# Kernel optimization log

Hardware: AMD Instinct MI355X
Metric: run time of the kernel (lower is better)

The kernel has to match this reference:

```python
import jax, jax.numpy as jnp
import numpy as np

N = 8192        # nodes (A.shape[0])
D_IN = 128      # input_dim
D_OUT = 128     # output_dim
D_THETA = 256   # hardcoded in GCN_liner_theta_1
DROP_KEEP = 0.8 # DropEdge percent


def setup_inputs() -> dict:
    key = jax.random.key(0)
    ks = jax.random.split(key, 6)
    H = jax.random.normal(ks[0], (N, D_IN), dtype=jnp.float32)
    U = jax.random.uniform(ks[1], (N, N), dtype=jnp.float32)
    upper = jnp.triu((U < 0.01).astype(jnp.float32), 1)
    A_adj = upper + upper.T + jnp.eye(N, dtype=jnp.float32)
    bn_gamma = jnp.ones((D_IN,), jnp.float32)
    bn_beta = jnp.zeros((D_IN,), jnp.float32)
    W_theta = jax.random.normal(ks[2], (D_THETA, D_IN), jnp.float32) * 0.05
    b_theta = jnp.zeros((D_THETA,), jnp.float32)
    W_out = jax.random.normal(ks[3], (D_OUT, D_IN), jnp.float32) * 0.05
    b_out = jnp.zeros((D_OUT,), jnp.float32)
    return {"H": H, "A_adj": A_adj, "bn_gamma": bn_gamma, "bn_beta": bn_beta,
            "W_theta": W_theta, "b_theta": b_theta, "W_out": W_out, "b_out": b_out}


def reference(H, A_adj, bn_gamma, bn_beta, W_theta, b_theta, W_out, b_out):
    n = H.shape[0]
    # BatchNorm1d in training mode: batch stats over the node dimension
    mean = H.mean(axis=0)
    var = H.var(axis=0)  # biased, matches torch training normalization
    Hn = (H - mean) * jax.lax.rsqrt(var + 1e-5) * bn_gamma + bn_beta

    # theta projection -> pairwise euclidean distances
    Hx = Hn @ W_theta.T + b_theta                     # [N, 256]
    sq = jnp.sum(Hx * Hx, axis=1)                     # [N]
    dist = sq[:, None] + sq[None, :] - 2.0 * (Hx @ Hx.T)
    dist = jnp.sqrt(jnp.clip(dist, 1e-12, None))      # [N, N]

    A = jnp.exp(-0.2 * dist)
    A = jnp.clip(jax.nn.sigmoid(A), 0.1, None)
    # DropEdge detaches A in the original (A never carries grad)
    A = jax.lax.stop_gradient(A)

    dkey = jax.random.key(42)
    keep = jax.random.uniform(dkey, (n, n)) < DROP_KEEP
    triu = jnp.triu(jnp.ones((n, n), dtype=bool), 0)
    Bt = jnp.where(triu & keep, A, 0.0)
    B = Bt + Bt.T - jnp.diag(jnp.diag(Bt))

    mask = jnp.ceil(A_adj * 1e-5)
    A2 = B * mask + jnp.eye(n, dtype=B.dtype)
    A3 = jnp.where(A2 > 0.6, A2, 0.0)                 # threshold (host loop in torch)

    # symmetric normalization D^-1/2 A D^-1/2 without dense diag matmuls
    d_inv_sqrt = jax.lax.rsqrt(A3.sum(axis=1))        # diag always >= 1
    A_hat = A3 * d_inv_sqrt[:, None] * d_inv_sqrt[None, :]

    out = A_hat @ (Hn @ W_out.T + b_out)              # [N, D_OUT]
    out = jnp.where(out >= 0, out, 0.01 * out)        # LeakyReLU(0.01)
    return out, A3
```

## Files before the change

### kernel.cpp

```cpp
#include <hip/hip_runtime.h>
#include <cstdint>
#include <cstddef>

#define N 8192
#define DIN 128
#define DTH 256
#define DOUT 128
#define ROWCAP 256
#define LISTCAP 512

__device__ __forceinline__ void threefry_0_42(uint32_t x0, uint32_t x1,
                                              uint32_t& o0, uint32_t& o1) {
  const uint32_t ks0 = 0u;
  const uint32_t ks1 = 42u;
  const uint32_t ks2 = 0x1BD11BDAu ^ 0u ^ 42u;
  x0 += ks0; x1 += ks1;
#define TF_R(r) { x0 += x1; x1 = (x1 << (r)) | (x1 >> (32 - (r))); x1 ^= x0; }
  TF_R(13) TF_R(15) TF_R(26) TF_R(6)
  x0 += ks1; x1 += ks2 + 1u;
  TF_R(17) TF_R(29) TF_R(16) TF_R(24)
  x0 += ks2; x1 += ks0 + 2u;
  TF_R(13) TF_R(15) TF_R(26) TF_R(6)
  x0 += ks0; x1 += ks1 + 3u;
  TF_R(17) TF_R(29) TF_R(16) TF_R(24)
  x0 += ks1; x1 += ks2 + 4u;
  TF_R(13) TF_R(15) TF_R(26) TF_R(6)
  x0 += ks2; x1 += ks0 + 5u;
#undef TF_R
  o0 = x0; o1 = x1;
}

__device__ __forceinline__ bool dropedge_keep(uint32_t t) {
  uint32_t y0, y1;
  threefry_0_42(0u, t, y0, y1);
  uint32_t bits = y0 ^ y1;
  float u = __uint_as_float((bits >> 9) | 0x3f800000u) - 1.0f;
  return u < 0.8f;
}

__global__ __launch_bounds__(256) void k_pre(
    const float* __restrict__ H,
    const float* __restrict__ Wt, const float* __restrict__ bt,
    const float* __restrict__ Wo, const float* __restrict__ bo,
    float* __restrict__ part_s, float* __restrict__ part_s2,
    float* __restrict__ Wc, float* __restrict__ bc,
    float* __restrict__ deg ) {
  int b = blockIdx.x;
  int tid = threadIdx.x;
  if (b < 64) {
    __shared__ float ls[8][DIN];
    __shared__ float ls2[8][DIN];
    int rg = tid >> 5;
    int c4 = tid & 31;
    int rbase = b * 128;
    float s[4] = {0,0,0,0}, s2[4] = {0,0,0,0};
    for (int k = 0; k < 16; ++k) {
      int r = rbase + rg + k * 8;
      float4 h = ((const float4*)(H + (size_t)r * DIN))[c4];
      s[0] += h.x; s2[0] += h.x * h.x;
      s[1] += h.y; s2[1] += h.y * h.y;
      s[2] += h.z; s2[2] += h.z * h.z;
      s[3] += h.w; s2[3] += h.w * h.w;
    }
#pragma unroll
    for (int q = 0; q < 4; ++q) { ls[rg][c4*4+q] = s[q]; ls2[rg][c4*4+q] = s2[q]; }
    __syncthreads();
    if (tid < DIN) {
      float a = 0.f, bb = 0.f;
#pragma unroll
      for (int g = 0; g < 8; ++g) { a += ls[g][tid]; bb += ls2[g][tid]; }
      part_s[b * DIN + tid] = a;
      part_s2[b * DIN + tid] = bb;
    }
  } else if (b < 256) {
    int idx = (b - 64) * 256 + tid;
    int k = idx / 384, c = idx % 384;
    Wc[idx] = (c < 256) ? Wt[(size_t)c * DIN + k] : Wo[(size_t)(c - 256) * DIN + k];
  } else if (b < 258) {
    int c = (b - 256) * 256 + tid;
    if (c < 384) bc[c] = (c < 256) ? bt[c] : bo[c - 256];
  } else {
    int g = (b - 258) * 256 + tid;
    ((int4*)deg)[g] = make_int4(0, 0, 0, 0);
  }
}

__global__ void k_bn_final(const float* __restrict__ part_s,
                           const float* __restrict__ part_s2,
                           const float* __restrict__ gamma,
                           const float* __restrict__ beta,
                           float* __restrict__ scale,
                           float* __restrict__ shift) {
  int c = threadIdx.x;
  float s = 0.f, s2 = 0.f;
  for (int b = 0; b < 64; ++b) { s += part_s[b*DIN+c]; s2 += part_s2[b*DIN+c]; }
  float mean = s * (1.0f / N);
  float var  = s2 * (1.0f / N) - mean * mean;
  float sc = rsqrtf(var + 1e-5f) * gamma[c];
  scale[c] = sc;
  shift[c] = beta[c] - mean * sc;
}

__device__ __forceinline__ unsigned short f2bf(float v) {
  uint32_t u = __float_as_uint(v);
  u += 0x7fffu + ((u >> 16) & 1u);
  return (unsigned short)(u >> 16);
}

__global__ __launch_bounds__(256) void k_rows(
    const float* __restrict__ H, const float* __restrict__ scale,
    const float* __restrict__ shift, const float* __restrict__ Wc,
    const float* __restrict__ bc, unsigned short* __restrict__ Hxh,
    float* __restrict__ HW, float* __restrict__ sq) {
  __shared__ float hn[16][DIN];
  int tid = threadIdx.x;
  int base = blockIdx.x * 16;
#pragma unroll
  for (int k = 0; k < 2; ++k) {
    int f = tid + k * 256;
    int r = f >> 5, c4 = f & 31;
    float4 h  = ((const float4*)(H + (size_t)(base + r) * DIN))[c4];
    float4 sc = ((const float4*)scale)[c4];
    float4 sh = ((const float4*)shift)[c4];
    h.x = h.x * sc.x + sh.x; h.y = h.y * sc.y + sh.y;
    h.z = h.z * sc.z + sh.z; h.w = h.w * sc.w + sh.w;
    ((float4*)hn[r])[c4] = h;
  }
  __syncthreads();
  int w = tid >> 6, lane = tid & 63;
  int r0 = w * 4;
  float acc[4][6];
#pragma unroll
  for (int r = 0; r < 4; ++r)
#pragma unroll
    for (int q = 0; q < 6; ++q) acc[r][q] = 0.f;

  for (int k4 = 0; k4 < 32; ++k4) {
    float4 h[4];
#pragma unroll
    for (int r = 0; r < 4; ++r) h[r] = ((const float4*)hn[r0 + r])[k4];
#pragma unroll
    for (int kk = 0; kk < 4; ++kk) {
      const float* wrow = Wc + (size_t)(k4 * 4 + kk) * 384 + lane;
      float wv[6];
#pragma unroll
      for (int q = 0; q < 6; ++q) wv[q] = wrow[64 * q];
#pragma unroll
      for (int r = 0; r < 4; ++r) {
        float hs = (kk == 0) ? h[r].x : (kk == 1) ? h[r].y
                 : (kk == 2) ? h[r].z : h[r].w;
#pragma unroll
        for (int q = 0; q < 6; ++q) acc[r][q] += hs * wv[q];
      }
    }
  }
#pragma unroll
  for (int r = 0; r < 4; ++r) {
    int row = base + r0 + r;
    float s = 0.f;
#pragma unroll
    for (int q = 0; q < 4; ++q) {
      float v = acc[r][q] + bc[lane + 64 * q];
      Hxh[(size_t)row * DTH + lane + 64 * q] = f2bf(v);
      s += v * v;
    }
#pragma unroll
    for (int off = 32; off > 0; off >>= 1) s += __shfl_xor(s, off, 64);
    if (lane == 0) sq[row] = s;
#pragma unroll
    for (int q = 4; q < 6; ++q) {
      float v = acc[r][q] + bc[lane + 64 * q];
      HW[(size_t)row * DOUT + lane + 64 * (q - 4)] = v;
    }
  }
}

__global__ __launch_bounds__(256) void k_main(
    const float* __restrict__ A_adj, const unsigned short* __restrict__ Hxh,
    const float* __restrict__ sq, float* __restrict__ A3,
    float* __restrict__ deg, int* __restrict__ nnz_cnt,
    int* __restrict__ nnz_idx, float* __restrict__ nnz_val) {
  int b = blockIdx.x;
  int tid = threadIdx.x;
  if (b < 8192) {
    float4* row = (float4*)(A3 + (size_t)b * N);
    const float4 z = make_float4(0.f, 0.f, 0.f, 0.f);
#pragma unroll
    for (int it = 0; it < 8; ++it) row[tid + it * 256] = z;
    return;
  }
  int i = b - 8192;
  __shared__ float4 hx4[64];
  __shared__ int   s_list[LISTCAP];
  __shared__ int   s_cnt;
  if (tid == 0) s_cnt = 0;
  ((float*)hx4)[tid] = __uint_as_float(((uint32_t)Hxh[(size_t)i * DTH + tid]) << 16);
  __syncthreads();

  const float4* arow = (const float4*)(A_adj + (size_t)i * N);
  int q0 = i >> 2;
  for (int q4 = q0 + tid; q4 < N / 4; q4 += 256) {
    float4 a = arow[q4];
    int jb = q4 * 4;
    float av[4] = {a.x, a.y, a.z, a.w};
#pragma unroll
    for (int q = 0; q < 4; ++q) {
      int j = jb + q;
      if (av[q] != 0.f && j >= i) {
        int p = atomicAdd(&s_cnt, 1);
        if (p < LISTCAP) s_list[p] = j;
      }
    }
  }
  __syncthreads();

  int M = min(s_cnt, LISTCAP);
  float sqi = sq[i];
  for (int t = tid; t < M; t += 256) {
    int j = s_list[t];
    bool keep = dropedge_keep((uint32_t)i * (uint32_t)N + (uint32_t)j);
    float dist;
    if (j == i) {
      dist = 1e-6f;
    } else {
      const uint4* hj = (const uint4*)(Hxh + (size_t)j * DTH);
      float dot = 0.f;
#pragma unroll 8
      for (int c = 0; c < 32; ++c) {
        uint4 u = hj[c];
        float4 f0 = hx4[2 * c], f1 = hx4[2 * c + 1];
        dot += __uint_as_float(u.x << 16) * f0.x
             + __uint_as_float(u.x & 0xffff0000u) * f0.y
             + __uint_as_float(u.y << 16) * f0.z
             + __uint_as_float(u.y & 0xffff0000u) * f0.w
             + __uint_as_float(u.z << 16) * f1.x
             + __uint_as_float(u.z & 0xffff0000u) * f1.y
             + __uint_as_float(u.w << 16) * f1.z
             + __uint_as_float(u.w & 0xffff0000u) * f1.w;
      }
      dist = sqrtf(fmaxf(sqi + sq[j] - 2.0f * dot, 1e-12f));
    }
    float aval = expf(-0.2f * dist);
    float sg = fmaxf(1.0f / (1.0f + expf(-aval)), 0.1f);
    float bb = keep ? sg : 0.0f;
    float a2 = bb + ((i == j) ? 1.0f : 0.0f);
    float a3v = (a2 > 0.6f) ? a2 : 0.0f;
    if (a3v != 0.f) {
      atomicAdd(&deg[i], a3v);
      int p = atomicAdd(&nnz_cnt[i], 1);
      if (p < ROWCAP) {
        nnz_idx[(size_t)i * ROWCAP + p] = j;
        nnz_val[(size_t)i * ROWCAP + p] = a3v;
      }
      if (j != i) {
        atomicAdd(&deg[j], a3v);
        int p2 = atomicAdd(&nnz_cnt[j], 1);
        if (p2 < ROWCAP) {
          nnz_idx[(size_t)j * ROWCAP + p2] = i;
          nnz_val[(size_t)j * ROWCAP + p2] = a3v;
        }
      }
    }
  }
}

__global__ __launch_bounds__(128) void k_post(
    const float* __restrict__ HW, const float* __restrict__ deg,
    const int* __restrict__ nnz_cnt, const int* __restrict__ nnz_idx,
    const float* __restrict__ nnz_val, float* __restrict__ A3,
    float* __restrict__ out) {
  int i = blockIdx.x;
  int c = threadIdx.x;
  int cnt = min(nnz_cnt[i], ROWCAP);
  for (int e = c; e < cnt; e += 128)
    A3[(size_t)i * N + nnz_idx[(size_t)i * ROWCAP + e]] =
        nnz_val[(size_t)i * ROWCAP + e];
  float acc = 0.f;
  for (int e = 0; e < cnt; ++e) {
    int j = nnz_idx[(size_t)i * ROWCAP + e];
    float v = nnz_val[(size_t)i * ROWCAP + e];
    acc += v * rsqrtf(deg[j]) * HW[(size_t)j * DOUT + c];
  }
  float o = rsqrtf(deg[i]) * acc;
  out[(size_t)i * DOUT + c] = (o >= 0.f) ? o : 0.01f * o;
}

extern "C" void kernel_launch(void* const* d_in, const int* in_sizes, int n_in,
                              void* d_out, int out_size, void* d_ws, size_t ws_size,
                              hipStream_t stream) {
  const float* H     = (const float*)d_in[0];
  const float* A_adj = (const float*)d_in[1];
  const float* gamma = (const float*)d_in[2];
  const float* beta  = (const float*)d_in[3];
  const float* Wt    = (const float*)d_in[4];
  const float* bt    = (const float*)d_in[5];
  const float* Wo    = (const float*)d_in[6];
  const float* bo    = (const float*)d_in[7];

  float* out = (float*)d_out;
  float* A3  = out + (size_t)N * DOUT;

  float* ws    = (float*)d_ws;
  float* scale = ws;
  float* shift = ws + 128;
  unsigned short* Hxh = (unsigned short*)(ws + 256);
  float* sq    = ws + 256 + (size_t)N * 128;
  float* HW    = sq + N;
  float* deg   = HW + (size_t)N * DOUT;
  int*   nnz_cnt = (int*)(deg + N);
  int*   nnz_idx = nnz_cnt + N;
  float* nnz_val = (float*)(nnz_idx + (size_t)N * ROWCAP);
  float* part_s  = nnz_val + (size_t)N * ROWCAP;
  float* part_s2 = part_s + 64 * DIN;
  float* Wc      = part_s2 + 64 * DIN;
  float* bc      = Wc + 128 * 384;

  k_pre<<<274, 256, 0, stream>>>(H, Wt, bt, Wo, bo, part_s, part_s2, Wc, bc, deg);
  k_bn_final<<<1, DIN, 0, stream>>>(part_s, part_s2, gamma, beta, scale, shift);
  k_rows<<<N / 16, 256, 0, stream>>>(H, scale, shift, Wc, bc, Hxh, HW, sq);
  k_main<<<2 * N, 256, 0, stream>>>(A_adj, Hxh, sq, A3, deg, nnz_cnt, nnz_idx, nnz_val);
  k_post<<<N, DOUT, 0, stream>>>(HW, deg, nnz_cnt, nnz_idx, nnz_val, A3, out);
}
```

Baseline: 492.1 us.

## Fold BN finalize into row kernel, move A3 zeroing earlier, scatter A3 in main

Removes the single-block BatchNorm finalize launch by having each k_rows block recompute scale and shift into shared memory. The dense A3 zero-fill moves from k_main into extra blocks of k_rows and uses nontemporal stores, and the adjacency row reads in k_main use nontemporal loads. Nonzero A3 entries are now written directly in k_main instead of being scattered in k_post. LISTCAP is halved to 256, which reduces shared memory use but raises the chance of the per-row candidate list overflowing on denser rows.

```diff
diff --git a/kernel.cpp b/kernel.cpp
--- a/kernel.cpp
+++ b/kernel.cpp
@@ -7,7 +7,9 @@
 #define DTH 256
 #define DOUT 128
 #define ROWCAP 256
-#define LISTCAP 512
+#define LISTCAP 256
+
+typedef float vfloat4 __attribute__((ext_vector_type(4)));
 
 __device__ __forceinline__ void threefry_0_42(uint32_t x0, uint32_t x1,
                                               uint32_t& o0, uint32_t& o1) {
@@ -36,6 +38,12 @@
   uint32_t bits = y0 ^ y1;
   float u = __uint_as_float((bits >> 9) | 0x3f800000u) - 1.0f;
   return u < 0.8f;
+}
+
+__device__ __forceinline__ unsigned short f2bf(float v) {
+  uint32_t u = __float_as_uint(v);
+  u += 0x7fffu + ((u >> 16) & 1u);
+  return (unsigned short)(u >> 16);
 }
 
 __global__ __launch_bounds__(256) void k_pre(
@@ -85,43 +93,44 @@
   }
 }
 
-__global__ void k_bn_final(const float* __restrict__ part_s,
-                           const float* __restrict__ part_s2,
-                           const float* __restrict__ gamma,
-                           const float* __restrict__ beta,
-                           float* __restrict__ scale,
-                           float* __restrict__ shift) {
-  int c = threadIdx.x;
-  float s = 0.f, s2 = 0.f;
-  for (int b = 0; b < 64; ++b) { s += part_s[b*DIN+c]; s2 += part_s2[b*DIN+c]; }
-  float mean = s * (1.0f / N);
-  float var  = s2 * (1.0f / N) - mean * mean;
-  float sc = rsqrtf(var + 1e-5f) * gamma[c];
-  scale[c] = sc;
-  shift[c] = beta[c] - mean * sc;
-}
-
-__device__ __forceinline__ unsigned short f2bf(float v) {
-  uint32_t u = __float_as_uint(v);
-  u += 0x7fffu + ((u >> 16) & 1u);
-  return (unsigned short)(u >> 16);
-}
-
 __global__ __launch_bounds__(256) void k_rows(
-    const float* __restrict__ H, const float* __restrict__ scale,
-    const float* __restrict__ shift, const float* __restrict__ Wc,
-    const float* __restrict__ bc, unsigned short* __restrict__ Hxh,
-    float* __restrict__ HW, float* __restrict__ sq) {
+    const float* __restrict__ H,
+    const float* __restrict__ part_s, const float* __restrict__ part_s2,
+    const float* __restrict__ gamma, const float* __restrict__ beta,
+    const float* __restrict__ Wc, const float* __restrict__ bc,
+    unsigned short* __restrict__ Hxh, float* __restrict__ HW,
+    float* __restrict__ sq, float* __restrict__ A3) {
+  int tid = threadIdx.x;
+  int b = blockIdx.x;
+  if (b >= 512) {
+    vfloat4* row = (vfloat4*)(A3 + (size_t)(b - 512) * N);
+    const vfloat4 z = {0.f, 0.f, 0.f, 0.f};
+#pragma unroll
+    for (int it = 0; it < 8; ++it)
+      __builtin_nontemporal_store(z, row + tid + it * 256);
+    return;
+  }
+  __shared__ __align__(16) float ssc[DIN];
+  __shared__ __align__(16) float ssh[DIN];
   __shared__ float hn[16][DIN];
-  int tid = threadIdx.x;
-  int base = blockIdx.x * 16;
+  if (tid < DIN) {
+    float s = 0.f, s2 = 0.f;
+    for (int g = 0; g < 64; ++g) { s += part_s[g*DIN+tid]; s2 += part_s2[g*DIN+tid]; }
+    float mean = s * (1.0f / N);
+    float var  = s2 * (1.0f / N) - mean * mean;
+    float sc = rsqrtf(var + 1e-5f) * gamma[tid];
+    ssc[tid] = sc;
+    ssh[tid] = beta[tid] - mean * sc;
+  }
+  __syncthreads();
+  int base = b * 16;
 #pragma unroll
   for (int k = 0; k < 2; ++k) {
     int f = tid + k * 256;
     int r = f >> 5, c4 = f & 31;
     float4 h  = ((const float4*)(H + (size_t)(base + r) * DIN))[c4];
-    float4 sc = ((const float4*)scale)[c4];
-    float4 sh = ((const float4*)shift)[c4];
+    float4 sc = ((const float4*)ssc)[c4];
+    float4 sh = ((const float4*)ssh)[c4];
     h.x = h.x * sc.x + sh.x; h.y = h.y * sc.y + sh.y;
     h.z = h.z * sc.z + sh.z; h.w = h.w * sc.w + sh.w;
     ((float4*)hn[r])[c4] = h;
@@ -180,16 +189,8 @@
     const float* __restrict__ sq, float* __restrict__ A3,
     float* __restrict__ deg, int* __restrict__ nnz_cnt,
     int* __restrict__ nnz_idx, float* __restrict__ nnz_val) {
-  int b = blockIdx.x;
+  int i = blockIdx.x;
   int tid = threadIdx.x;
-  if (b < 8192) {
-    float4* row = (float4*)(A3 + (size_t)b * N);
-    const float4 z = make_float4(0.f, 0.f, 0.f, 0.f);
-#pragma unroll
-    for (int it = 0; it < 8; ++it) row[tid + it * 256] = z;
-    return;
-  }
-  int i = b - 8192;
   __shared__ float4 hx4[64];
   __shared__ int   s_list[LISTCAP];
   __shared__ int   s_cnt;
@@ -197,10 +198,10 @@
   ((float*)hx4)[tid] = __uint_as_float(((uint32_t)Hxh[(size_t)i * DTH + tid]) << 16);
   __syncthreads();
 
-  const float4* arow = (const float4*)(A_adj + (size_t)i * N);
+  const vfloat4* arow = (const vfloat4*)(A_adj + (size_t)i * N);
   int q0 = i >> 2;
   for (int q4 = q0 + tid; q4 < N / 4; q4 += 256) {
-    float4 a = arow[q4];
+    vfloat4 a = __builtin_nontemporal_load(arow + q4);
     int jb = q4 * 4;
     float av[4] = {a.x, a.y, a.z, a.w};
 #pragma unroll
@@ -246,6 +247,7 @@
     float a2 = bb + ((i == j) ? 1.0f : 0.0f);
     float a3v = (a2 > 0.6f) ? a2 : 0.0f;
     if (a3v != 0.f) {
+      A3[(size_t)i * N + j] = a3v;
       atomicAdd(&deg[i], a3v);
       int p = atomicAdd(&nnz_cnt[i], 1);
       if (p < ROWCAP) {
@@ -253,6 +255,7 @@
         nnz_val[(size_t)i * ROWCAP + p] = a3v;
       }
       if (j != i) {
+        A3[(size_t)j * N + i] = a3v;
         atomicAdd(&deg[j], a3v);
         int p2 = atomicAdd(&nnz_cnt[j], 1);
         if (p2 < ROWCAP) {
@@ -267,14 +270,10 @@
 __global__ __launch_bounds__(128) void k_post(
     const float* __restrict__ HW, const float* __restrict__ deg,
     const int* __restrict__ nnz_cnt, const int* __restrict__ nnz_idx,
-    const float* __restrict__ nnz_val, float* __restrict__ A3,
-    float* __restrict__ out) {
+    const float* __restrict__ nnz_val, float* __restrict__ out) {
   int i = blockIdx.x;
   int c = threadIdx.x;
   int cnt = min(nnz_cnt[i], ROWCAP);
-  for (int e = c; e < cnt; e += 128)
-    A3[(size_t)i * N + nnz_idx[(size_t)i * ROWCAP + e]] =
-        nnz_val[(size_t)i * ROWCAP + e];
   float acc = 0.f;
   for (int e = 0; e < cnt; ++e) {
     int j = nnz_idx[(size_t)i * ROWCAP + e];
@@ -301,10 +300,8 @@
   float* A3  = out + (size_t)N * DOUT;
 
   float* ws    = (float*)d_ws;
-  float* scale = ws;
-  float* shift = ws + 128;
-  unsigned short* Hxh = (unsigned short*)(ws + 256);
-  float* sq    = ws + 256 + (size_t)N * 128;
+  unsigned short* Hxh = (unsigned short*)ws;
+  float* sq    = ws + (size_t)N * 128;
   float* HW    = sq + N;
   float* deg   = HW + (size_t)N * DOUT;
   int*   nnz_cnt = (int*)(deg + N);
@@ -316,8 +313,8 @@
   float* bc      = Wc + 128 * 384;
 
   k_pre<<<274, 256, 0, stream>>>(H, Wt, bt, Wo, bo, part_s, part_s2, Wc, bc, deg);
-  k_bn_final<<<1, DIN, 0, stream>>>(part_s, part_s2, gamma, beta, scale, shift);
-  k_rows<<<N / 16, 256, 0, stream>>>(H, scale, shift, Wc, bc, Hxh, HW, sq);
-  k_main<<<2 * N, 256, 0, stream>>>(A_adj, Hxh, sq, A3, deg, nnz_cnt, nnz_idx, nnz_val);
-  k_post<<<N, DOUT, 0, stream>>>(HW, deg, nnz_cnt, nnz_idx, nnz_val, A3, out);
-}
+  k_rows<<<512 + N, 256, 0, stream>>>(H, part_s, part_s2, gamma, beta, Wc, bc,
+                                      Hxh, HW, sq, A3);
+  k_main<<<N, 256, 0, stream>>>(A_adj, Hxh, sq, A3, deg, nnz_cnt, nnz_idx, nnz_val);
+  k_post<<<N, DOUT, 0, stream>>>(HW, deg, nnz_cnt, nnz_idx, nnz_val, out);
+}
```

After: 461.4 us (median of 2 runs). -6.2%, faster.
